# Kernel optimization log

Hardware: AMD Instinct MI355X
Metric: run time of the kernel (lower is better)

The kernel has to match this reference:

```python
import jax, jax.numpy as jnp
import numpy as np
from jax import lax

NUM_CLASSES = 4   # includes ignore label 0
IGNORE = 0
MAX_SAMPLES = 1024
HALF = MAX_SAMPLES // 2
BIG = 1 << 30     # sentinel key for invalid/unselected pixels


def setup_inputs() -> dict:
    key = jax.random.key(0)
    k1, k2, k3 = jax.random.split(key, 3)
    B, C, H, W = 4, 64, 256, 256
    feat_map = jax.random.normal(k1, (B, C, H, W), dtype=jnp.float32)
    labels = jax.random.randint(k2, (B, H, W), 0, NUM_CLASSES, dtype=jnp.int32)
    preds = jax.random.normal(k3, (B, NUM_CLASSES, H, W), dtype=jnp.float32)
    return {"feat_map": feat_map, "labels": labels, "preds": preds}


def _soft_dilate2d(x):
    # F.max_pool2d(x, kernel=3, stride=1, padding=1) on [B,1,H,W]
    return lax.reduce_window(x, -jnp.inf, lax.max, (1, 1, 3, 3), (1, 1, 1, 1), "SAME")


def _per_pair(fm, lab, pd, cls):
    # fm: [C, N] features, lab: [N] int labels, pd: [N] dilated pred class, cls: scalar int
    N = lab.shape[0]
    ar = jnp.arange(N)
    clsf = cls.astype(pd.dtype)
    in_cls = lab == cls
    hard = (pd != clsf) & in_cls   # mispredicted (after dilation) pixels of this class
    easy = (pd == clsf) & in_cls
    # torch code uses randperm; reference uses the deterministic identity
    # permutation: keep the first HALF hard pixels (in raster order).
    hard_key = jnp.where(hard, ar, BIG)
    hard_top = jnp.sort(hard_key)[:HALF]                      # [HALF]
    valid_h = (hard_top < BIG).astype(fm.dtype)
    feat_h = fm[:, jnp.where(hard_top < BIG, hard_top, 0)] * valid_h  # [C, HALF], zero-padded
    # rest pool = leftover hard pixels (rank >= HALF) first, then easy pixels;
    # keep first HALF of that concatenation.
    hard_rank = jnp.cumsum(hard) - 1
    easy_rank = jnp.cumsum(easy) - 1
    excess = jnp.maximum(jnp.sum(hard) - HALF, 0)
    rest_key = jnp.where(hard & (hard_rank >= HALF), hard_rank - HALF,
                         jnp.where(easy, excess + easy_rank, BIG))
    order = jnp.argsort(rest_key)[:HALF]                      # pixel indices, valid first
    valid_r = (jnp.take(rest_key, order) < BIG).astype(fm.dtype)
    feat_r = fm[:, order] * valid_r                           # [C, HALF], zero-padded
    return jnp.concatenate([feat_h, feat_r], axis=1)          # [C, MAX_SAMPLES]


def reference(feat_map, labels, preds):
    B, C, H, W = feat_map.shape
    N = H * W
    # softmax preserves argmax -> skip the softmax
    pred_lab = jnp.argmax(preds, axis=1).astype(feat_map.dtype)[:, None]  # [B,1,H,W]
    preds_d = _soft_dilate2d(pred_lab).reshape(B, N)
    feat_flat = feat_map.reshape(B, C, N)
    lab_flat = labels.reshape(B, N)
    # assume all non-ignore classes present in each image (true w.h.p. for
    # random labels over 65536 pixels) -> static total_classes = B*(NUM_CLASSES-1)
    b_idx = jnp.repeat(jnp.arange(B), NUM_CLASSES - 1)
    cls_idx = jnp.tile(jnp.arange(1, NUM_CLASSES), B)
    feat_extract = jax.vmap(_per_pair)(feat_flat[b_idx], lab_flat[b_idx],
                                       preds_d[b_idx], cls_idx)  # [B*(NC-1), C, 1024]
    feat_label = cls_idx.astype(jnp.float32)
    return feat_extract, feat_label
```

## Files before the change

kernel.cpp:

```cpp
#include <hip/hip_runtime.h>

#define BB 4
#define CC 64
#define HH 256
#define WW 256
#define NPIX (HH*WW)
#define NCLS 4
#define NPAIR 12
#define HALF 512
#define MAXS 1024
#define CHUNK 4096
#define NCHUNK (NPIX/CHUNK)
#define TPB 256
#define PXT (CHUNK/TPB)

__global__ void k_argmax(const float* __restrict__ preds, unsigned char* __restrict__ amax) {
    int i = blockIdx.x * blockDim.x + threadIdx.x;
    if (i >= BB * NPIX) return;
    int b = i >> 16;
    int pix = i & (NPIX - 1);
    const float* p = preds + (size_t)b * NCLS * NPIX + pix;
    float best = p[0];
    int arg = 0;
#pragma unroll
    for (int c = 1; c < NCLS; ++c) {
        float v = p[(size_t)c * NPIX];
        if (v > best) { best = v; arg = c; }
    }
    amax[i] = (unsigned char)arg;
}

__global__ void k_dilate(const unsigned char* __restrict__ amax, unsigned char* __restrict__ pd) {
    int i = blockIdx.x * blockDim.x + threadIdx.x;
    if (i >= BB * NPIX) return;
    int b = i >> 16;
    int pix = i & (NPIX - 1);
    int y = pix >> 8;
    int x = pix & (WW - 1);
    const unsigned char* base = amax + b * NPIX;
    int mv = 0;
    for (int dy = -1; dy <= 1; ++dy) {
        int yy = y + dy;
        if (yy < 0 || yy >= HH) continue;
        for (int dx = -1; dx <= 1; ++dx) {
            int xx = x + dx;
            if (xx < 0 || xx >= WW) continue;
            int v = base[yy * WW + xx];
            if (v > mv) mv = v;
        }
    }
    pd[i] = (unsigned char)mv;
}

__global__ void k_count(const int* __restrict__ labels, const unsigned char* __restrict__ pd,
                        unsigned* __restrict__ chunkCounts) {
    int pair = blockIdx.x, chunk = blockIdx.y, t = threadIdx.x;
    int b = pair / 3, cls = pair % 3 + 1;
    const int* lab = labels + b * NPIX;
    const unsigned char* p = pd + b * NPIX;
    int start = chunk * CHUNK + t * PXT;
    int hc = 0, ec = 0;
#pragma unroll
    for (int j = 0; j < PXT; ++j) {
        int pix = start + j;
        int l = lab[pix];
        int d = p[pix];
        if (l == cls) { if (d == cls) ec++; else hc++; }
    }
    __shared__ unsigned s[TPB];
    s[t] = (unsigned)hc | ((unsigned)ec << 16);
    __syncthreads();
    for (int off = TPB / 2; off > 0; off >>= 1) {
        if (t < off) s[t] += s[t + off];
        __syncthreads();
    }
    if (t == 0) chunkCounts[pair * NCHUNK + chunk] = s[0];
}

__global__ void k_scan(const unsigned* __restrict__ chunkCounts, int2* __restrict__ chunkBases,
                       int* __restrict__ hardTotals, int* __restrict__ slots) {
    int t = threadIdx.x;
    if (t < NPAIR) {
        int hb = 0, eb = 0;
        for (int ch = 0; ch < NCHUNK; ++ch) {
            unsigned v = chunkCounts[t * NCHUNK + ch];
            chunkBases[t * NCHUNK + ch] = make_int2(hb, eb);
            hb += (int)(v & 0xffffu);
            eb += (int)(v >> 16);
        }
        hardTotals[t] = hb;
    }
    for (int i = t; i < NPAIR * MAXS; i += blockDim.x) slots[i] = -1;
}

__global__ void k_assign(const int* __restrict__ labels, const unsigned char* __restrict__ pd,
                         const int2* __restrict__ chunkBases, const int* __restrict__ hardTotals,
                         int* __restrict__ slots) {
    int pair = blockIdx.x, chunk = blockIdx.y, t = threadIdx.x;
    int b = pair / 3, cls = pair % 3 + 1;
    const int* lab = labels + b * NPIX;
    const unsigned char* p = pd + b * NPIX;
    int start = chunk * CHUNK + t * PXT;
    int hc = 0, ec = 0;
#pragma unroll
    for (int j = 0; j < PXT; ++j) {
        int pix = start + j;
        int l = lab[pix];
        int d = p[pix];
        if (l == cls) { if (d == cls) ec++; else hc++; }
    }
    __shared__ unsigned s[TPB];
    unsigned mine = (unsigned)hc | ((unsigned)ec << 16);
    s[t] = mine;
    __syncthreads();
    for (int off = 1; off < TPB; off <<= 1) {
        unsigned v = (t >= off) ? s[t - off] : 0u;
        __syncthreads();
        s[t] += v;
        __syncthreads();
    }
    unsigned excl = s[t] - mine;
    int2 base = chunkBases[pair * NCHUNK + chunk];
    int hr = base.x + (int)(excl & 0xffffu);
    int er = base.y + (int)(excl >> 16);
    int excess = hardTotals[pair] - HALF;
    if (excess < 0) excess = 0;
    int* sl = slots + pair * MAXS;
#pragma unroll
    for (int j = 0; j < PXT; ++j) {
        int pix = start + j;
        int l = lab[pix];
        int d = p[pix];
        if (l == cls) {
            if (d != cls) {
                if (hr < MAXS) sl[hr] = pix;
                hr++;
            } else {
                int pos = HALF + excess + er;
                if (pos < MAXS) sl[pos] = pix;
                er++;
            }
        }
    }
}

__global__ void k_gather(const float* __restrict__ feat, const int* __restrict__ slots,
                         float* __restrict__ out) {
    int i = blockIdx.x * blockDim.x + threadIdx.x;
    const int NOUT = NPAIR * CC * MAXS;
    if (i < NOUT) {
        int pair = i / (CC * MAXS);
        int c = (i >> 10) & (CC - 1);
        int slot = i & (MAXS - 1);
        int pix = slots[pair * MAXS + slot];
        int b = pair / 3;
        out[i] = (pix >= 0) ? feat[((size_t)(b * CC + c)) * NPIX + pix] : 0.0f;
    } else if (i < NOUT + NPAIR) {
        int pair = i - NOUT;
        out[i] = (float)(pair % 3 + 1);
    }
}

extern "C" void kernel_launch(void* const* d_in, const int* in_sizes, int n_in,
                              void* d_out, int out_size, void* d_ws, size_t ws_size,
                              hipStream_t stream) {
    const float* feat   = (const float*)d_in[0];
    const int*   labels = (const int*)d_in[1];
    const float* preds  = (const float*)d_in[2];
    float* out = (float*)d_out;

    unsigned char* amax = (unsigned char*)d_ws;
    unsigned char* pd   = amax + BB * NPIX;
    unsigned* chunkCounts = (unsigned*)(pd + BB * NPIX);
    int2* chunkBases = (int2*)(chunkCounts + NPAIR * NCHUNK);
    int* hardTotals = (int*)(chunkBases + NPAIR * NCHUNK);
    int* slots = hardTotals + NPAIR;

    int npx = BB * NPIX;
    k_argmax<<<npx / 256, 256, 0, stream>>>(preds, amax);
    k_dilate<<<npx / 256, 256, 0, stream>>>(amax, pd);
    dim3 g(NPAIR, NCHUNK);
    k_count<<<g, TPB, 0, stream>>>(labels, pd, chunkCounts);
    k_scan<<<1, 256, 0, stream>>>(chunkCounts, chunkBases, hardTotals, slots);
    k_assign<<<g, TPB, 0, stream>>>(labels, pd, chunkBases, hardTotals, slots);
    int nout = NPAIR * CC * MAXS + NPAIR;
    k_gather<<<(nout + 255) / 256, 256, 0, stream>>>(feat, slots, out);
}
```

Before: 117.8 us.

## Fuse argmax with dilation, collapse count/scan/assign into one block per pair

Argmax and the 3x3 max dilation are merged into one tiled kernel that computes argmax into a shared-memory halo tile and then dilates from it. The separate count, scan and assign kernels become a single 1024-thread block per pair that counts, scans with wave shuffles, and writes slots through shared memory. The gather is changed to emit float4 outputs. This cuts kernel launches and global round trips, but each compaction block now scans a whole image serially with only 12 blocks, and each thread reads 64 strided pixels, which may coalesce poorly.

```diff
diff --git a/kernel.cpp b/kernel.cpp
--- a/kernel.cpp
+++ b/kernel.cpp
@@ -9,130 +9,94 @@
 #define NPAIR 12
 #define HALF 512
 #define MAXS 1024
-#define CHUNK 4096
-#define NCHUNK (NPIX/CHUNK)
-#define TPB 256
-#define PXT (CHUNK/TPB)
+#define NOUT (NPAIR*CC*MAXS)
 
-__global__ void k_argmax(const float* __restrict__ preds, unsigned char* __restrict__ amax) {
-    int i = blockIdx.x * blockDim.x + threadIdx.x;
-    if (i >= BB * NPIX) return;
-    int b = i >> 16;
-    int pix = i & (NPIX - 1);
-    const float* p = preds + (size_t)b * NCLS * NPIX + pix;
-    float best = p[0];
-    int arg = 0;
+__global__ void k_dargmax(const float* __restrict__ preds, unsigned char* __restrict__ pd) {
+    __shared__ unsigned char tile[18][18];
+    int b = blockIdx.z;
+    int ty0 = blockIdx.y * 16, tx0 = blockIdx.x * 16;
+    const float* pb = preds + (size_t)b * NCLS * NPIX;
+    for (int i = threadIdx.x; i < 18 * 18; i += 256) {
+        int hy = i / 18, hx = i - hy * 18;
+        int y = ty0 + hy - 1, x = tx0 + hx - 1;
+        unsigned char a = 0;
+        if (y >= 0 && y < HH && x >= 0 && x < WW) {
+            const float* p = pb + y * WW + x;
+            float best = p[0];
+            int arg = 0;
 #pragma unroll
-    for (int c = 1; c < NCLS; ++c) {
-        float v = p[(size_t)c * NPIX];
-        if (v > best) { best = v; arg = c; }
+            for (int c = 1; c < NCLS; ++c) {
+                float v = p[(size_t)c * NPIX];
+                if (v > best) { best = v; arg = c; }
+            }
+            a = (unsigned char)arg;
+        }
+        tile[hy][hx] = a;
     }
-    amax[i] = (unsigned char)arg;
+    __syncthreads();
+    int ly = threadIdx.x >> 4, lx = threadIdx.x & 15;
+    int mv = 0;
+#pragma unroll
+    for (int dy = 0; dy < 3; ++dy)
+#pragma unroll
+        for (int dx = 0; dx < 3; ++dx) {
+            int v = tile[ly + dy][lx + dx];
+            if (v > mv) mv = v;
+        }
+    pd[b * NPIX + (ty0 + ly) * WW + (tx0 + lx)] = (unsigned char)mv;
 }
 
-__global__ void k_dilate(const unsigned char* __restrict__ amax, unsigned char* __restrict__ pd) {
-    int i = blockIdx.x * blockDim.x + threadIdx.x;
-    if (i >= BB * NPIX) return;
-    int b = i >> 16;
-    int pix = i & (NPIX - 1);
-    int y = pix >> 8;
-    int x = pix & (WW - 1);
-    const unsigned char* base = amax + b * NPIX;
-    int mv = 0;
-    for (int dy = -1; dy <= 1; ++dy) {
-        int yy = y + dy;
-        if (yy < 0 || yy >= HH) continue;
-        for (int dx = -1; dx <= 1; ++dx) {
-            int xx = x + dx;
-            if (xx < 0 || xx >= WW) continue;
-            int v = base[yy * WW + xx];
-            if (v > mv) mv = v;
-        }
-    }
-    pd[i] = (unsigned char)mv;
-}
-
-__global__ void k_count(const int* __restrict__ labels, const unsigned char* __restrict__ pd,
-                        unsigned* __restrict__ chunkCounts) {
-    int pair = blockIdx.x, chunk = blockIdx.y, t = threadIdx.x;
+__global__ void __launch_bounds__(1024) k_compact(
+        const int* __restrict__ labels, const unsigned char* __restrict__ pd,
+        int* __restrict__ slots, float* __restrict__ out) {
+    int pair = blockIdx.x;
     int b = pair / 3, cls = pair % 3 + 1;
     const int* lab = labels + b * NPIX;
     const unsigned char* p = pd + b * NPIX;
-    int start = chunk * CHUNK + t * PXT;
+    int t = threadIdx.x;
+    int lane = t & 63, w = t >> 6;
+
+    __shared__ int sl[MAXS];
+    __shared__ unsigned waveSums[16];
+    sl[t] = -1;
+
+    int start = t * 64;
     int hc = 0, ec = 0;
+#pragma unroll 8
+    for (int j = 0; j < 64; ++j) {
+        int pix = start + j;
+        if (lab[pix] == cls) { if (p[pix] == cls) ec++; else hc++; }
+    }
+    unsigned mine = (unsigned)hc | ((unsigned)ec << 16);
+
+    unsigned v = mine;
 #pragma unroll
-    for (int j = 0; j < PXT; ++j) {
+    for (int off = 1; off < 64; off <<= 1) {
+        unsigned u = (unsigned)__shfl_up((int)v, off, 64);
+        if (lane >= off) v += u;
+    }
+    if (lane == 63) waveSums[w] = v;
+    __syncthreads();
+    if (t == 0) {
+        unsigned acc = 0;
+#pragma unroll
+        for (int i = 0; i < 16; ++i) { acc += waveSums[i]; waveSums[i] = acc; }
+    }
+    __syncthreads();
+    unsigned waveBase = (w > 0) ? waveSums[w - 1] : 0u;
+    unsigned total = waveSums[15];
+    unsigned excl = waveBase + v - mine;
+
+    int hr = (int)(excl & 0xffffu);
+    int er = (int)(excl >> 16);
+    int excess = (int)(total & 0xffffu) - HALF;
+    if (excess < 0) excess = 0;
+
+#pragma unroll 8
+    for (int j = 0; j < 64; ++j) {
         int pix = start + j;
-        int l = lab[pix];
-        int d = p[pix];
-        if (l == cls) { if (d == cls) ec++; else hc++; }
-    }
-    __shared__ unsigned s[TPB];
-    s[t] = (unsigned)hc | ((unsigned)ec << 16);
-    __syncthreads();
-    for (int off = TPB / 2; off > 0; off >>= 1) {
-        if (t < off) s[t] += s[t + off];
-        __syncthreads();
-    }
-    if (t == 0) chunkCounts[pair * NCHUNK + chunk] = s[0];
-}
-
-__global__ void k_scan(const unsigned* __restrict__ chunkCounts, int2* __restrict__ chunkBases,
-                       int* __restrict__ hardTotals, int* __restrict__ slots) {
-    int t = threadIdx.x;
-    if (t < NPAIR) {
-        int hb = 0, eb = 0;
-        for (int ch = 0; ch < NCHUNK; ++ch) {
-            unsigned v = chunkCounts[t * NCHUNK + ch];
-            chunkBases[t * NCHUNK + ch] = make_int2(hb, eb);
-            hb += (int)(v & 0xffffu);
-            eb += (int)(v >> 16);
-        }
-        hardTotals[t] = hb;
-    }
-    for (int i = t; i < NPAIR * MAXS; i += blockDim.x) slots[i] = -1;
-}
-
-__global__ void k_assign(const int* __restrict__ labels, const unsigned char* __restrict__ pd,
-                         const int2* __restrict__ chunkBases, const int* __restrict__ hardTotals,
-                         int* __restrict__ slots) {
-    int pair = blockIdx.x, chunk = blockIdx.y, t = threadIdx.x;
-    int b = pair / 3, cls = pair % 3 + 1;
-    const int* lab = labels + b * NPIX;
-    const unsigned char* p = pd + b * NPIX;
-    int start = chunk * CHUNK + t * PXT;
-    int hc = 0, ec = 0;
-#pragma unroll
-    for (int j = 0; j < PXT; ++j) {
-        int pix = start + j;
-        int l = lab[pix];
-        int d = p[pix];
-        if (l == cls) { if (d == cls) ec++; else hc++; }
-    }
-    __shared__ unsigned s[TPB];
-    unsigned mine = (unsigned)hc | ((unsigned)ec << 16);
-    s[t] = mine;
-    __syncthreads();
-    for (int off = 1; off < TPB; off <<= 1) {
-        unsigned v = (t >= off) ? s[t - off] : 0u;
-        __syncthreads();
-        s[t] += v;
-        __syncthreads();
-    }
-    unsigned excl = s[t] - mine;
-    int2 base = chunkBases[pair * NCHUNK + chunk];
-    int hr = base.x + (int)(excl & 0xffffu);
-    int er = base.y + (int)(excl >> 16);
-    int excess = hardTotals[pair] - HALF;
-    if (excess < 0) excess = 0;
-    int* sl = slots + pair * MAXS;
-#pragma unroll
-    for (int j = 0; j < PXT; ++j) {
-        int pix = start + j;
-        int l = lab[pix];
-        int d = p[pix];
-        if (l == cls) {
-            if (d != cls) {
+        if (lab[pix] == cls) {
+            if (p[pix] != cls) {
                 if (hr < MAXS) sl[hr] = pix;
                 hr++;
             } else {
@@ -142,23 +106,30 @@
             }
         }
     }
+    __syncthreads();
+    slots[pair * MAXS + t] = sl[t];
+    if (t == 0) out[NOUT + pair] = (float)cls;
 }
 
 __global__ void k_gather(const float* __restrict__ feat, const int* __restrict__ slots,
                          float* __restrict__ out) {
     int i = blockIdx.x * blockDim.x + threadIdx.x;
-    const int NOUT = NPAIR * CC * MAXS;
-    if (i < NOUT) {
-        int pair = i / (CC * MAXS);
-        int c = (i >> 10) & (CC - 1);
-        int slot = i & (MAXS - 1);
-        int pix = slots[pair * MAXS + slot];
-        int b = pair / 3;
-        out[i] = (pix >= 0) ? feat[((size_t)(b * CC + c)) * NPIX + pix] : 0.0f;
-    } else if (i < NOUT + NPAIR) {
-        int pair = i - NOUT;
-        out[i] = (float)(pair % 3 + 1);
-    }
+    const int NQ = NOUT / 4;
+    if (i >= NQ) return;
+    int q = i << 2;
+    int pair = q >> 16;
+    int c = (q >> 10) & (CC - 1);
+    int slot = q & (MAXS - 1);
+    int b = pair / 3;
+    const float* fp = feat + ((size_t)(b * CC + c)) * NPIX;
+    const int* sp = slots + pair * MAXS + slot;
+    int p0 = sp[0], p1 = sp[1], p2 = sp[2], p3 = sp[3];
+    float4 o;
+    o.x = (p0 >= 0) ? fp[p0] : 0.0f;
+    o.y = (p1 >= 0) ? fp[p1] : 0.0f;
+    o.z = (p2 >= 0) ? fp[p2] : 0.0f;
+    o.w = (p3 >= 0) ? fp[p3] : 0.0f;
+    ((float4*)out)[i] = o;
 }
 
 extern "C" void kernel_launch(void* const* d_in, const int* in_sizes, int n_in,
@@ -169,20 +140,11 @@
     const float* preds  = (const float*)d_in[2];
     float* out = (float*)d_out;
 
-    unsigned char* amax = (unsigned char*)d_ws;
-    unsigned char* pd   = amax + BB * NPIX;
-    unsigned* chunkCounts = (unsigned*)(pd + BB * NPIX);
-    int2* chunkBases = (int2*)(chunkCounts + NPAIR * NCHUNK);
-    int* hardTotals = (int*)(chunkBases + NPAIR * NCHUNK);
-    int* slots = hardTotals + NPAIR;
+    unsigned char* pd = (unsigned char*)d_ws;
+    int* slots = (int*)(pd + BB * NPIX);
 
-    int npx = BB * NPIX;
-    k_argmax<<<npx / 256, 256, 0, stream>>>(preds, amax);
-    k_dilate<<<npx / 256, 256, 0, stream>>>(amax, pd);
-    dim3 g(NPAIR, NCHUNK);
-    k_count<<<g, TPB, 0, stream>>>(labels, pd, chunkCounts);
-    k_scan<<<1, 256, 0, stream>>>(chunkCounts, chunkBases, hardTotals, slots);
-    k_assign<<<g, TPB, 0, stream>>>(labels, pd, chunkBases, hardTotals, slots);
-    int nout = NPAIR * CC * MAXS + NPAIR;
-    k_gather<<<(nout + 255) / 256, 256, 0, stream>>>(feat, slots, out);
+    dim3 g1(WW / 16, HH / 16, BB);
+    k_dargmax<<<g1, 256, 0, stream>>>(preds, pd);
+    k_compact<<<NPAIR, 1024, 0, stream>>>(labels, pd, slots, out);
+    k_gather<<<(NOUT / 4 + 255) / 256, 256, 0, stream>>>(feat, slots, out);
 }
```

Result: slower. 176.9 us (+50.2%).
